# Kernel tuning notes

Hardware: AMD Instinct MI355X
Metric: run time of the kernel (lower is better)

The kernel has to match this reference:

```python
import jax, jax.numpy as jnp
import numpy as np
import math

B, L, D, H, F = 4, 2048, 1024, 16, 4096
SF = 5          # sampling_factor
EPS = 1e-12     # LayerNorm eps


def setup_inputs() -> dict:
    key = jax.random.key(0)
    ks = jax.random.split(key, 18)
    s = 0.02
    lin = lambda k, i, o: (jax.random.normal(k, (i, o), jnp.float32) * s)
    log_LK = math.ceil(math.log1p(L))
    U_part = min(SF * L * log_LK, L)  # = L here
    return {
        "x": jax.random.normal(ks[0], (B, L, D), jnp.float32),
        "wq": lin(ks[1], D, D), "bq": jnp.zeros((D,), jnp.float32),
        "wk": lin(ks[2], D, D), "bk": jnp.zeros((D,), jnp.float32),
        "wv": lin(ks[3], D, D), "bv": jnp.zeros((D,), jnp.float32),
        "wo": lin(ks[4], D, D), "bo": jnp.zeros((D,), jnp.float32),
        "w1": lin(ks[5], D, F), "b1": jnp.zeros((F,), jnp.float32),
        "w2": lin(ks[6], F, D), "b2": jnp.zeros((D,), jnp.float32),
        "gamma1": jnp.ones((D,), jnp.float32), "beta1": jnp.zeros((D,), jnp.float32),
        "gamma2": jnp.ones((D,), jnp.float32), "beta2": jnp.zeros((D,), jnp.float32),
        "index_sample": jax.random.randint(ks[7], (U_part,), 0, L, jnp.int32),
    }


def _layernorm(x, g, b):
    m = x.mean(-1, keepdims=True)
    v = ((x - m) ** 2).mean(-1, keepdims=True)  # unbiased=False
    return g * (x - m) / jnp.sqrt(v + EPS) + b


def _prob_sparse_mha(x, wq, bq, wk, bk, wv, bv, wo, bo, index_sample):
    d = D // H
    BH = B * H
    # NOTE: source views q as (B, H, L, d) WITHOUT transpose (quirk kept);
    # k, v are split with the usual (B, L, H, d) -> (B, H, L, d) transpose.
    q = (x @ wq + bq).reshape(BH, L, d)
    k = (x @ wk + bk).reshape(B, L, H, d).transpose(0, 2, 1, 3).reshape(BH, L, d)
    v = (x @ wv + bv).reshape(B, L, H, d).transpose(0, 2, 1, 3).reshape(BH, L, d)

    # --- ProbSparse query selection ---
    K_sample = k[:, index_sample, :]                       # [BH, U_part, d]
    QK = jnp.einsum('bqd,bkd->bqk', q, K_sample)           # [BH, L, U_part]
    M = QK.max(axis=-1) - QK.sum(axis=-1) / L              # sparsity measure
    u = min(SF * math.ceil(math.log1p(L)), L)              # static: 40
    _, M_top = jax.lax.top_k(-M, u)                        # largest=False in src
    Q_reduce = jnp.take_along_axis(q, M_top[:, :, None], axis=1)  # [BH, u, d]

    # --- attention for the selected queries ---
    scores = jnp.einsum('bud,bkd->buk', Q_reduce, k) / math.sqrt(d)
    probs = jax.nn.softmax(scores, axis=-1)
    out_red = jnp.einsum('buk,bkd->bud', probs, v)         # [BH, u, d]

    # scatter reduced outputs back to full length (non-selected rows -> 0)
    full = jnp.zeros_like(q).at[jnp.arange(BH)[:, None], M_top].set(out_red)
    out = full.reshape(B, H, L, d).transpose(0, 2, 1, 3).reshape(B, L, D)
    return out @ wo + bo


def reference(x, wq, bq, wk, bk, wv, bv, wo, bo, w1, b1, w2, b2,
              gamma1, beta1, gamma2, beta2, index_sample):
    a = _prob_sparse_mha(x, wq, bq, wk, bk, wv, bv, wo, bo, index_sample)
    x1 = _layernorm(x + a, gamma1, beta1)          # dropout = identity (eval)
    f = jnp.maximum(x1 @ w1 + b1, 0.0) @ w2 + b2   # FFN (ReLU)
    return _layernorm(x1 + f, gamma2, beta2)
```

## Files before the change

### kernel.cpp

```cpp
#include <hip/hip_runtime.h>
#include <float.h>
#include <math.h>

#define L_SEQ 2048
#define D_MODEL 1024
#define N_HEAD 16
#define HD 64
#define N_BH 64
#define U_TOP 40

using bf16x8 = __attribute__((ext_vector_type(8))) short;
using f32x4  = __attribute__((ext_vector_type(4))) float;

__device__ __forceinline__ unsigned short f2bf(float f) {
    unsigned int u = __builtin_bit_cast(unsigned int, f);
    u += 0x7fff + ((u >> 16) & 1);
    return (unsigned short)(u >> 16);
}
__device__ __forceinline__ float bf2f(unsigned short h) {
    unsigned int u = ((unsigned int)h) << 16;
    return __builtin_bit_cast(float, u);
}

__device__ __forceinline__ void gload_lds16(const void* g, void* l) {
    __builtin_amdgcn_global_load_lds(
        (const __attribute__((address_space(1))) unsigned int*)g,
        (__attribute__((address_space(3))) unsigned int*)l, 16, 0, 0);
}

template<bool OUTBF16, bool RELU, bool ACCUM>
__global__ void __launch_bounds__(256)
gemm_bf16(const unsigned short* __restrict__ A, int lda,
          const unsigned short* __restrict__ BT, int ldbt,
          void* __restrict__ Cp, int ldc, int K,
          const float* __restrict__ bias)
{
    __shared__ short As[4096];
    __shared__ short Bs[4096];
    const int tid = threadIdx.x;
    const int w = tid >> 6, l = tid & 63;
    const int bx = blockIdx.x, by = blockIdx.y;
    const int wm = w >> 1, wn = w & 1;

    f32x4 acc[4][4] = {};

    const unsigned short* a_src[2];
    const unsigned short* b_src[2];
#pragma unroll
    for (int g = 0; g < 2; ++g) {
        int r = w * 32 + g * 16 + (l >> 2);
        int kc = (l & 3) ^ ((r >> 1) & 3);
        a_src[g] = A + (size_t)(by * 128 + r) * lda + kc * 8;
        b_src[g] = BT + (size_t)(bx * 128 + r) * ldbt + kc * 8;
    }
    short* As_w = As + w * 1024;
    short* Bs_w = Bs + w * 1024;

    const int lr = l & 15, lg = l >> 4;

    for (int k0 = 0; k0 < K; k0 += 32) {
        __syncthreads();
        gload_lds16(a_src[0] + k0, As_w);
        gload_lds16(a_src[1] + k0, As_w + 512);
        gload_lds16(b_src[0] + k0, Bs_w);
        gload_lds16(b_src[1] + k0, Bs_w + 512);
        __syncthreads();

        bf16x8 af[4], bg[4];
#pragma unroll
        for (int m = 0; m < 4; ++m) {
            int row = wm * 64 + m * 16 + lr;
            int off = row * 64 + ((lg ^ ((row >> 1) & 3)) << 4);
            af[m] = *(const bf16x8*)((const char*)As + off);
        }
#pragma unroll
        for (int n = 0; n < 4; ++n) {
            int row = wn * 64 + n * 16 + lr;
            int off = row * 64 + ((lg ^ ((row >> 1) & 3)) << 4);
            bg[n] = *(const bf16x8*)((const char*)Bs + off);
        }
#pragma unroll
        for (int m = 0; m < 4; ++m)
#pragma unroll
            for (int n = 0; n < 4; ++n)
                acc[m][n] = __builtin_amdgcn_mfma_f32_16x16x32_bf16(
                    af[m], bg[n], acc[m][n], 0, 0, 0);
    }

    float bcol[4];
#pragma unroll
    for (int n = 0; n < 4; ++n) {
        int colg = bx * 128 + wn * 64 + n * 16 + lr;
        bcol[n] = bias ? bias[colg] : 0.f;
    }
#pragma unroll
    for (int m = 0; m < 4; ++m) {
#pragma unroll
        for (int n = 0; n < 4; ++n) {
            int colg = bx * 128 + wn * 64 + n * 16 + lr;
#pragma unroll
            for (int r = 0; r < 4; ++r) {
                int rowg = by * 128 + wm * 64 + m * 16 + lg * 4 + r;
                float v = acc[m][n][r] + bcol[n];
                if (RELU) v = fmaxf(v, 0.f);
                if (OUTBF16) {
                    ((unsigned short*)Cp)[(size_t)rowg * ldc + colg] = f2bf(v);
                } else {
                    float* C = (float*)Cp;
                    if (ACCUM) v += C[(size_t)rowg * ldc + colg];
                    C[(size_t)rowg * ldc + colg] = v;
                }
            }
        }
    }
}

__global__ void __launch_bounds__(256)
gemm_bf16_split(const unsigned short* __restrict__ Ah,
                const unsigned short* __restrict__ Al, int lda,
                const unsigned short* __restrict__ BhT,
                const unsigned short* __restrict__ BlT, int ldbt,
                unsigned short* __restrict__ CP, int K,
                const float* __restrict__ bias)
{
    __shared__ short Ash[4096], Asl[4096], Bsh[4096], Bsl[4096];
    const int tid = threadIdx.x;
    const int w = tid >> 6, l = tid & 63;
    const int bx = blockIdx.x, by = blockIdx.y;
    const int wm = w >> 1, wn = w & 1;

    f32x4 acc[4][4] = {};

    size_t a_off[2], b_off[2];
#pragma unroll
    for (int g = 0; g < 2; ++g) {
        int r = w * 32 + g * 16 + (l >> 2);
        int kc = (l & 3) ^ ((r >> 1) & 3);
        a_off[g] = (size_t)(by * 128 + r) * lda + kc * 8;
        b_off[g] = (size_t)(bx * 128 + r) * ldbt + kc * 8;
    }
    const int wb = w * 1024;
    const int lr = l & 15, lg = l >> 4;

    for (int k0 = 0; k0 < K; k0 += 32) {
        __syncthreads();
#pragma unroll
        for (int g = 0; g < 2; ++g) {
            gload_lds16(Ah + a_off[g] + k0, Ash + wb + g * 512);
            gload_lds16(Al + a_off[g] + k0, Asl + wb + g * 512);
            gload_lds16(BhT + b_off[g] + k0, Bsh + wb + g * 512);
            gload_lds16(BlT + b_off[g] + k0, Bsl + wb + g * 512);
        }
        __syncthreads();

        bf16x8 afh[4], afl[4], bgh[4], bgl[4];
#pragma unroll
        for (int m = 0; m < 4; ++m) {
            int row = wm * 64 + m * 16 + lr;
            int off = row * 64 + ((lg ^ ((row >> 1) & 3)) << 4);
            afh[m] = *(const bf16x8*)((const char*)Ash + off);
            afl[m] = *(const bf16x8*)((const char*)Asl + off);
        }
#pragma unroll
        for (int n = 0; n < 4; ++n) {
            int row = wn * 64 + n * 16 + lr;
            int off = row * 64 + ((lg ^ ((row >> 1) & 3)) << 4);
            bgh[n] = *(const bf16x8*)((const char*)Bsh + off);
            bgl[n] = *(const bf16x8*)((const char*)Bsl + off);
        }
#pragma unroll
        for (int m = 0; m < 4; ++m)
#pragma unroll
            for (int n = 0; n < 4; ++n) {
                acc[m][n] = __builtin_amdgcn_mfma_f32_16x16x32_bf16(
                    afh[m], bgh[n], acc[m][n], 0, 0, 0);
                acc[m][n] = __builtin_amdgcn_mfma_f32_16x16x32_bf16(
                    afh[m], bgl[n], acc[m][n], 0, 0, 0);
                acc[m][n] = __builtin_amdgcn_mfma_f32_16x16x32_bf16(
                    afl[m], bgh[n], acc[m][n], 0, 0, 0);
            }
    }

    float bcol[4];
#pragma unroll
    for (int n = 0; n < 4; ++n)
        bcol[n] = bias[bx * 128 + wn * 64 + n * 16 + lr];
    const int cg = bx * 2 + wn;
#pragma unroll
    for (int m = 0; m < 4; ++m)
#pragma unroll
        for (int n = 0; n < 4; ++n) {
            int cwi = n * 16 + lr;
#pragma unroll
            for (int r = 0; r < 4; ++r) {
                int rowg = by * 128 + wm * 64 + m * 16 + lg * 4 + r;
                float v = acc[m][n][r] + bcol[n];
                unsigned short hh = f2bf(v);
                unsigned short ll = f2bf(v - bf2f(hh));
                size_t ad = (size_t)rowg * 2048 + cg * 128 + cwi;
                CP[ad] = hh;
                CP[ad + 64] = ll;
            }
        }
}

__global__ void __launch_bounds__(256)
gather_ks(const unsigned short* __restrict__ KP, const int* __restrict__ idxs,
          unsigned short* __restrict__ KS)
{
    const int bh = blockIdx.x, b = bh >> 4, h = bh & 15;
    const int r0 = blockIdx.y * 256;
    const int s = threadIdx.x & 15, jr = threadIdx.x >> 4;
#pragma unroll
    for (int p = 0; p < 16; ++p) {
        int j = r0 + p * 16 + jr;
        int idx = idxs[j];
        int kc = (s & 7) ^ (j & 7);
        const unsigned short* src = KP + (size_t)(b * 2048 + idx) * 2048
                                  + h * 128 + ((s & 8) << 3) + kc * 8;
        *(bf16x8*)(KS + ((size_t)bh * 2048 + j) * 128 + s * 8) =
            *(const bf16x8*)src;
    }
}

__global__ void __launch_bounds__(256)
mstat_mfma2(const unsigned short* __restrict__ QP,
            const unsigned short* __restrict__ KS,
            float* __restrict__ Mout)
{
    __shared__ char lds[32768];
    const int tid = threadIdx.x, w = tid >> 6, l = tid & 63;
    const int bh = blockIdx.x, qt = blockIdx.y;
    const int i0 = qt * 256;
    const int lr = l & 15, lg = l >> 4;

    bf16x8 af[4][2][2];
#pragma unroll
    for (int half = 0; half < 2; ++half) {
        __syncthreads();
#pragma unroll
        for (int it = 0; it < 8; ++it) {
            int rq = w * 64 + it * 8 + (l >> 3);
            int i = i0 + rq;
            int kc = (l & 7) ^ (rq & 7);
            gload_lds16(QP + (size_t)(bh * 128 + (i >> 4)) * 2048
                           + (i & 15) * 128 + half * 64 + kc * 8,
                        lds + w * 8192 + it * 1024);
        }
        __syncthreads();
#pragma unroll
        for (int m = 0; m < 4; ++m) {
            int rq = w * 64 + m * 16 + lr;
#pragma unroll
            for (int ks = 0; ks < 2; ++ks) {
                int c = (ks * 4 + lg) ^ (rq & 7);
                af[m][ks][half] = *(const bf16x8*)(lds + rq * 128 + (c << 4));
            }
        }
    }
    __syncthreads();

    float mx[4][4], sm[4][4];
#pragma unroll
    for (int m = 0; m < 4; ++m)
#pragma unroll
        for (int r = 0; r < 4; ++r) { mx[m][r] = -FLT_MAX; sm[m][r] = 0.f; }

    const unsigned short* ksbase = KS + (size_t)bh * (2048 * 128);

#pragma unroll
    for (int it = 0; it < 4; ++it)
        gload_lds16(ksbase + w * 2048 + it * 512 + l * 8,
                    lds + w * 4096 + it * 1024);

    for (int jt = 0; jt < 32; ++jt) {
        const int cur = jt & 1;
        __syncthreads();
        if (jt + 1 < 32) {
#pragma unroll
            for (int it = 0; it < 4; ++it)
                gload_lds16(ksbase + (size_t)(jt + 1) * 8192 + w * 2048 + it * 512 + l * 8,
                            lds + (cur ^ 1) * 16384 + w * 4096 + it * 1024);
        }
        const char* kb = lds + cur * 16384;
#pragma unroll
        for (int n = 0; n < 4; ++n) {
            int jr = n * 16 + lr;
            bf16x8 bgh[2], bgl[2];
#pragma unroll
            for (int ks = 0; ks < 2; ++ks) {
                int c = (ks * 4 + lg) ^ (jr & 7);
                bgh[ks] = *(const bf16x8*)(kb + jr * 256 + (c << 4));
                bgl[ks] = *(const bf16x8*)(kb + jr * 256 + (c << 4) + 128);
            }
#pragma unroll
            for (int m = 0; m < 4; ++m) {
                f32x4 a = {};
                a = __builtin_amdgcn_mfma_f32_16x16x32_bf16(af[m][0][0], bgh[0], a, 0, 0, 0);
                a = __builtin_amdgcn_mfma_f32_16x16x32_bf16(af[m][0][1], bgh[0], a, 0, 0, 0);
                a = __builtin_amdgcn_mfma_f32_16x16x32_bf16(af[m][0][0], bgl[0], a, 0, 0, 0);
                a = __builtin_amdgcn_mfma_f32_16x16x32_bf16(af[m][1][0], bgh[1], a, 0, 0, 0);
                a = __builtin_amdgcn_mfma_f32_16x16x32_bf16(af[m][1][1], bgh[1], a, 0, 0, 0);
                a = __builtin_amdgcn_mfma_f32_16x16x32_bf16(af[m][1][0], bgl[1], a, 0, 0, 0);
#pragma unroll
                for (int r = 0; r < 4; ++r) {
                    mx[m][r] = fmaxf(mx[m][r], a[r]);
                    sm[m][r] += a[r];
                }
            }
        }
    }

#pragma unroll
    for (int m = 0; m < 4; ++m)
#pragma unroll
        for (int r = 0; r < 4; ++r) {
            float a = mx[m][r], s = sm[m][r];
#pragma unroll
            for (int mask = 1; mask < 16; mask <<= 1) {
                a = fmaxf(a, __shfl_xor(a, mask));
                s += __shfl_xor(s, mask);
            }
            if (lr == 0) {
                int row = i0 + w * 64 + m * 16 + lg * 4 + r;
                Mout[(size_t)bh * L_SEQ + row] = a - s * (1.0f / 2048.0f);
            }
        }
}

__global__ void __launch_bounds__(256)
tconv(const float* __restrict__ in, int R, int C, unsigned short* __restrict__ out)
{
    __shared__ float t[32][33];
    const int bx = blockIdx.x * 32;
    const int by = blockIdx.y * 32;
    const int lx = threadIdx.x & 31, ly = threadIdx.x >> 5;
#pragma unroll
    for (int r = 0; r < 4; ++r)
        t[ly + r * 8][lx] = in[(size_t)(by + ly + r * 8) * C + bx + lx];
    __syncthreads();
#pragma unroll
    for (int r = 0; r < 4; ++r) {
        int oc = ly + r * 8;
        out[(size_t)(bx + oc) * R + by + lx] = f2bf(t[lx][oc]);
    }
}

__global__ void __launch_bounds__(256)
tconv_split(const float* __restrict__ in, int R, int C,
            unsigned short* __restrict__ outh, unsigned short* __restrict__ outl)
{
    __shared__ float t[32][33];
    const int bx = blockIdx.x * 32;
    const int by = blockIdx.y * 32;
    const int lx = threadIdx.x & 31, ly = threadIdx.x >> 5;
#pragma unroll
    for (int r = 0; r < 4; ++r)
        t[ly + r * 8][lx] = in[(size_t)(by + ly + r * 8) * C + bx + lx];
    __syncthreads();
#pragma unroll
    for (int r = 0; r < 4; ++r) {
        int oc = ly + r * 8;
        float f = t[lx][oc];
        unsigned short hh = f2bf(f);
        outh[(size_t)(bx + oc) * R + by + lx] = hh;
        outl[(size_t)(bx + oc) * R + by + lx] = f2bf(f - bf2f(hh));
    }
}

__global__ void __launch_bounds__(256)
split_f32(const float* __restrict__ in, unsigned short* __restrict__ hi,
          unsigned short* __restrict__ lo)
{
    size_t i = ((size_t)blockIdx.x * 256 + threadIdx.x) * 4;
    float4 v = *(const float4*)(in + i);
    ushort4 h, l2;
    h.x = f2bf(v.x); l2.x = f2bf(v.x - bf2f(h.x));
    h.y = f2bf(v.y); l2.y = f2bf(v.y - bf2f(h.y));
    h.z = f2bf(v.z); l2.z = f2bf(v.z - bf2f(h.z));
    h.w = f2bf(v.w); l2.w = f2bf(v.w - bf2f(h.w));
    *(ushort4*)(hi + i) = h;
    *(ushort4*)(lo + i) = l2;
}

__global__ void __launch_bounds__(256)
topk_kernel(const float* __restrict__ M, int* __restrict__ Mtop)
{
    __shared__ float mv[L_SEQ];
    __shared__ float wv_[4];
    __shared__ int wi_[4];
    const int bh = blockIdx.x;
    const int tid = threadIdx.x;
    for (int j = tid; j < L_SEQ; j += 256) mv[j] = M[(size_t)bh * L_SEQ + j];
    __syncthreads();
    for (int u = 0; u < U_TOP; ++u) {
        float best = FLT_MAX;
        int bi = 1 << 30;
        for (int j = tid; j < L_SEQ; j += 256) {
            float v = mv[j];
            if (v < best || (v == best && j < bi)) { best = v; bi = j; }
        }
#pragma unroll
        for (int off = 32; off; off >>= 1) {
            float ov = __shfl_down(best, off);
            int oi = __shfl_down(bi, off);
            if (ov < best || (ov == best && oi < bi)) { best = ov; bi = oi; }
        }
        if ((tid & 63) == 0) { wv_[tid >> 6] = best; wi_[tid >> 6] = bi; }
        __syncthreads();
        if (tid == 0) {
            for (int w = 1; w < 4; ++w)
                if (wv_[w] < best || (wv_[w] == best && wi_[w] < bi)) { best = wv_[w]; bi = wi_[w]; }
            Mtop[bh * U_TOP + u] = bi;
            mv[bi] = FLT_MAX;
        }
        __syncthreads();
    }
}

__global__ void __launch_bounds__(256)
attn_fused(const unsigned short* __restrict__ QP,
           const unsigned short* __restrict__ KP,
           const unsigned short* __restrict__ V,
           const int* __restrict__ Mtop,
           unsigned short* __restrict__ OUTC)
{
    __shared__ unsigned short Qs[64 * 64];
    __shared__ unsigned short Ks[128 * 64];
    __shared__ unsigned short Vt[64 * 128];
    __shared__ unsigned short Pb[64 * 128];
    const int bh = blockIdx.x;
    const int b = bh >> 4, h = bh & 15;
    const int tid = threadIdx.x, w = tid >> 6, l = tid & 63;
    const int lr = l & 15, lg = l >> 4;

#pragma unroll
    for (int is = 0; is < 2; ++is) {
        int row = w * 16 + is * 8 + (l >> 3);
        int u = row < U_TOP ? row : U_TOP - 1;
        int lsel = Mtop[bh * U_TOP + u];
        int cg = (l & 7) ^ (row & 7);
        gload_lds16(QP + (size_t)(bh * 128 + (lsel >> 4)) * 2048
                       + (lsel & 15) * 128 + cg * 8,
                    &Qs[(w * 16 + is * 8) * 64]);
    }
    __syncthreads();

    bf16x8 af[2];
    {
        int row = w * 16 + lr;
#pragma unroll
        for (int ks = 0; ks < 2; ++ks) {
            int c = (ks * 4 + lg) ^ (row & 7);
            af[ks] = *(const bf16x8*)((const char*)Qs + row * 128 + (c << 4));
        }
    }

    float m_run[4], l_run[4];
    f32x4 oacc[4] = {};
#pragma unroll
    for (int r = 0; r < 4; ++r) { m_run[r] = -FLT_MAX; l_run[r] = 0.f; }

    for (int t = 0; t < 16; ++t) {
        const int j0 = t * 128;
        __syncthreads();

#pragma unroll
        for (int is = 0; is < 4; ++is) {
            int kr = w * 32 + is * 8 + (l >> 3);
            int cg = (l & 7) ^ (kr & 7);
            gload_lds16(KP + (size_t)(b * 2048 + j0 + kr) * 2048 + h * 128 + cg * 8,
                        &Ks[(w * 32 + is * 8) * 64]);
        }
        {
            int key = tid & 127, dh = (tid >> 7) * 32;
            const unsigned short* vsrc =
                V + (((size_t)(b * L_SEQ + j0 + key)) << 10) + (h << 6) + dh;
            bf16x8 vv[4];
#pragma unroll
            for (int i = 0; i < 4; ++i) vv[i] = *(const bf16x8*)(vsrc + i * 8);
            int ck = key >> 3, klo = (key & 7) * 2;
#pragma unroll
            for (int i = 0; i < 4; ++i)
#pragma unroll
                for (int j = 0; j < 8; ++j) {
                    int d = dh + i * 8 + j;
                    *(unsigned short*)((char*)Vt + d * 256 +
                                       ((ck ^ (d & 7)) << 4) + klo) =
                        (unsigned short)vv[i][j];
                }
        }
        __syncthreads();

        f32x4 sc[8] = {};
#pragma unroll
        for (int ks = 0; ks < 2; ++ks)
#pragma unroll
            for (int n = 0; n < 8; ++n) {
                int krow = n * 16 + lr;
                int c = (ks * 4 + lg) ^ (krow & 7);
                bf16x8 bf = *(const bf16x8*)((const char*)Ks + krow * 128 + (c << 4));
                sc[n] = __builtin_amdgcn_mfma_f32_16x16x32_bf16(af[ks], bf, sc[n], 0, 0, 0);
            }

        float rs[4];
#pragma unroll
        for (int r = 0; r < 4; ++r) {
            int row = w * 16 + lg * 4 + r;
            float mt = -FLT_MAX;
#pragma unroll
            for (int n = 0; n < 8; ++n) mt = fmaxf(mt, sc[n][r]);
            mt *= 0.125f;
#pragma unroll
            for (int mask = 1; mask < 16; mask <<= 1)
                mt = fmaxf(mt, __shfl_xor(mt, mask));
            float mn = fmaxf(m_run[r], mt);
            rs[r] = expf(m_run[r] - mn);
            float ls = 0.f;
            int rsw = row & 7;
#pragma unroll
            for (int n = 0; n < 8; ++n) {
                float p = expf(sc[n][r] * 0.125f - mn);
                ls += p;
                int ckp = (lr >> 3) + 2 * n;
                *(unsigned short*)((char*)Pb + row * 256 +
                                   ((ckp ^ rsw) << 4) + (lr & 7) * 2) = f2bf(p);
            }
#pragma unroll
            for (int mask = 1; mask < 16; mask <<= 1) ls += __shfl_xor(ls, mask);
            l_run[r] = l_run[r] * rs[r] + ls;
            m_run[r] = mn;
        }
        __syncthreads();

#pragma unroll
        for (int n = 0; n < 4; ++n)
#pragma unroll
            for (int r = 0; r < 4; ++r) oacc[n][r] *= rs[r];
#pragma unroll
        for (int ks = 0; ks < 4; ++ks) {
            int arow = w * 16 + lr;
            int ca = (lg + ks * 4) ^ (arow & 7);
            bf16x8 pa = *(const bf16x8*)((const char*)Pb + arow * 256 + (ca << 4));
#pragma unroll
            for (int n = 0; n < 4; ++n) {
                int d = n * 16 + lr;
                int cb = (lg + ks * 4) ^ (d & 7);
                bf16x8 vb = *(const bf16x8*)((const char*)Vt + d * 256 + (cb << 4));
                oacc[n] = __builtin_amdgcn_mfma_f32_16x16x32_bf16(pa, vb, oacc[n], 0, 0, 0);
            }
        }
    }

#pragma unroll
    for (int r = 0; r < 4; ++r) {
        int row = w * 16 + lg * 4 + r;
        float inv = 1.f / l_run[r];
#pragma unroll
        for (int n = 0; n < 4; ++n)
            OUTC[bh * 4096 + row * 64 + n * 16 + lr] = f2bf(oacc[n][r] * inv);
    }
}

__global__ void __launch_bounds__(256)
woscatter(const unsigned short* __restrict__ OUTC,
          const unsigned short* __restrict__ woT,
          const int* __restrict__ Mtop,
          float* __restrict__ Ab)
{
    const int bh = blockIdx.x, b = bh >> 4, h = bh & 15;
    const int tid = threadIdx.x, w = tid >> 6, l = tid & 63;
    const int lr = l & 15, lg = l >> 4;

    bf16x8 af[3][2];
#pragma unroll
    for (int m = 0; m < 3; ++m)
#pragma unroll
        for (int ks = 0; ks < 2; ++ks)
            af[m][ks] = *(const bf16x8*)(OUTC + bh * 4096 + (m * 16 + lr) * 64
                                         + (ks * 4 + lg) * 8);
    int lsel[3][4];
#pragma unroll
    for (int m = 0; m < 3; ++m)
#pragma unroll
        for (int r = 0; r < 4; ++r) {
            int row = m * 16 + lg * 4 + r;
            lsel[m][r] = row < U_TOP ? Mtop[bh * U_TOP + row] : -1;
        }

    for (int nn = 0; nn < 16; ++nn) {
        int ng = w * 16 + nn;
        bf16x8 bg[2];
#pragma unroll
        for (int ks = 0; ks < 2; ++ks)
            bg[ks] = *(const bf16x8*)(woT + (size_t)(ng * 16 + lr) * 1024
                                      + h * 64 + (ks * 4 + lg) * 8);
        f32x4 a[3] = {};
#pragma unroll
        for (int m = 0; m < 3; ++m)
#pragma unroll
            for (int ks = 0; ks < 2; ++ks)
                a[m] = __builtin_amdgcn_mfma_f32_16x16x32_bf16(af[m][ks], bg[ks], a[m], 0, 0, 0);
#pragma unroll
        for (int m = 0; m < 3; ++m)
#pragma unroll
            for (int r = 0; r < 4; ++r)
                if (lsel[m][r] >= 0)
                    atomicAdd(Ab + (size_t)(b * 2048 + lsel[m][r]) * 1024
                              + ng * 16 + lr, a[m][r]);
    }
}

template<bool WB16, bool BADD>
__global__ void __launch_bounds__(256)
ln_kernel(const float* __restrict__ X, const float* __restrict__ A,
          const float* __restrict__ badd,
          const float* __restrict__ g, const float* __restrict__ be,
          float* __restrict__ out, unsigned short* __restrict__ out16)
{
    __shared__ float wred[4];
    const int row = blockIdx.x, tid = threadIdx.x;
    float4 xv = *(const float4*)(X + (size_t)row * D_MODEL + tid * 4);
    float4 av = *(const float4*)(A + (size_t)row * D_MODEL + tid * 4);
    float v0 = xv.x + av.x, v1 = xv.y + av.y, v2 = xv.z + av.z, v3 = xv.w + av.w;
    if (BADD) {
        float4 bb = *(const float4*)(badd + tid * 4);
        v0 += bb.x; v1 += bb.y; v2 += bb.z; v3 += bb.w;
    }

    float s = v0 + v1 + v2 + v3;
#pragma unroll
    for (int off = 32; off; off >>= 1) s += __shfl_down(s, off);
    if ((tid & 63) == 0) wred[tid >> 6] = s;
    __syncthreads();
    float mean = (wred[0] + wred[1] + wred[2] + wred[3]) * (1.f / 1024.f);
    __syncthreads();

    float d0 = v0 - mean, d1 = v1 - mean, d2 = v2 - mean, d3 = v3 - mean;
    float q = d0 * d0 + d1 * d1 + d2 * d2 + d3 * d3;
#pragma unroll
    for (int off = 32; off; off >>= 1) q += __shfl_down(q, off);
    if ((tid & 63) == 0) wred[tid >> 6] = q;
    __syncthreads();
    float var = (wred[0] + wred[1] + wred[2] + wred[3]) * (1.f / 1024.f);
    float rstd = rsqrtf(var + 1e-12f);

    float4 gv = *(const float4*)(g + tid * 4);
    float4 bv = *(const float4*)(be + tid * 4);
    float4 o;
    o.x = gv.x * d0 * rstd + bv.x;
    o.y = gv.y * d1 * rstd + bv.y;
    o.z = gv.z * d2 * rstd + bv.z;
    o.w = gv.w * d3 * rstd + bv.w;
    *(float4*)(out + (size_t)row * D_MODEL + tid * 4) = o;
    if (WB16) {
        ushort4 ob;
        ob.x = f2bf(o.x); ob.y = f2bf(o.y); ob.z = f2bf(o.z); ob.w = f2bf(o.w);
        *(ushort4*)(out16 + (size_t)row * D_MODEL + tid * 4) = ob;
    }
}

extern "C" void kernel_launch(void* const* d_in, const int* in_sizes, int n_in,
                              void* d_out, int out_size, void* d_ws, size_t ws_size,
                              hipStream_t stream)
{
    const float* x   = (const float*)d_in[0];
    const float* wq  = (const float*)d_in[1];
    const float* bq  = (const float*)d_in[2];
    const float* wk  = (const float*)d_in[3];
    const float* bk  = (const float*)d_in[4];
    const float* wv  = (const float*)d_in[5];
    const float* bv  = (const float*)d_in[6];
    const float* wo  = (const float*)d_in[7];
    const float* bo  = (const float*)d_in[8];
    const float* w1  = (const float*)d_in[9];
    const float* b1  = (const float*)d_in[10];
    const float* w2  = (const float*)d_in[11];
    const float* b2  = (const float*)d_in[12];
    const float* g1  = (const float*)d_in[13];
    const float* be1 = (const float*)d_in[14];
    const float* g2  = (const float*)d_in[15];
    const float* be2 = (const float*)d_in[16];
    const int*  idxs = (const int*)d_in[17];

    char* ws  = (char*)d_ws;
    char* dob = (char*)d_out;
    const size_t MB = 1u << 20;

    unsigned short* QP   = (unsigned short*)(ws);
    unsigned short* KP   = (unsigned short*)(ws + 32 * MB);
    unsigned short* xh   = (unsigned short*)(ws + 64 * MB);
    unsigned short* xl   = (unsigned short*)(ws + 80 * MB);
    unsigned short* KS   = (unsigned short*)(ws + 64 * MB);
    float*          Ab   = (float*)(ws + 64 * MB);
    float*          x1f  = (float*)(ws + 96 * MB);
    unsigned short* x1b  = (unsigned short*)(ws);
    unsigned short* w1T  = (unsigned short*)(ws + 16 * MB);
    unsigned short* w2T  = (unsigned short*)(ws + 24 * MB);
    unsigned short* HIDc = (unsigned short*)(ws + 32 * MB);

    unsigned short* woT  = (unsigned short*)(dob);
    unsigned short* wqhT = (unsigned short*)(dob + 2 * MB);
    unsigned short* wqlT = (unsigned short*)(dob + 4 * MB);
    unsigned short* wkhT = (unsigned short*)(dob + 6 * MB);
    unsigned short* wklT = (unsigned short*)(dob + 8 * MB);
    unsigned short* wvT  = (unsigned short*)(dob + 10 * MB);
    float*          Mb   = (float*)(dob + 12 * MB);
    int*            Mtop = (int*)(dob + 12 * MB + 768 * 1024);
    unsigned short* Vb   = (unsigned short*)(dob + 13 * MB);
    unsigned short* OUTC = (unsigned short*)(dob + 29 * MB);
    float*          F    = (float*)d_out;

    dim3 blk(256);
    dim3 g_gemm(8, 64);

    split_f32<<<dim3(8192), blk, 0, stream>>>(x, xh, xl);
    tconv_split<<<dim3(32, 32), blk, 0, stream>>>(wq, 1024, 1024, wqhT, wqlT);
    tconv_split<<<dim3(32, 32), blk, 0, stream>>>(wk, 1024, 1024, wkhT, wklT);
    tconv<<<dim3(32, 32), blk, 0, stream>>>(wv, 1024, 1024, wvT);
    tconv<<<dim3(32, 32), blk, 0, stream>>>(wo, 1024, 1024, woT);

    gemm_bf16_split<<<g_gemm, blk, 0, stream>>>(xh, xl, 1024, wqhT, wqlT, 1024,
                                                QP, 1024, bq);
    gemm_bf16_split<<<g_gemm, blk, 0, stream>>>(xh, xl, 1024, wkhT, wklT, 1024,
                                                KP, 1024, bk);
    gemm_bf16<true, false, false><<<g_gemm, blk, 0, stream>>>(xh, 1024, wvT, 1024,
                                                              Vb, 1024, 1024, bv);

    gather_ks<<<dim3(64, 8), blk, 0, stream>>>(KP, idxs, KS);
    mstat_mfma2<<<dim3(64, 8), blk, 0, stream>>>(QP, KS, Mb);
    topk_kernel<<<dim3(64), blk, 0, stream>>>(Mb, Mtop);

    hipMemsetAsync(Ab, 0, 32 * MB, stream);
    attn_fused<<<dim3(N_BH), blk, 0, stream>>>(QP, KP, Vb, Mtop, OUTC);
    woscatter<<<dim3(N_BH), blk, 0, stream>>>(OUTC, woT, Mtop, Ab);

    ln_kernel<true, true><<<dim3(8192), blk, 0, stream>>>(x, Ab, bo, g1, be1, x1f, x1b);

    tconv<<<dim3(128, 32), blk, 0, stream>>>(w1, 1024, 4096, w1T);
    tconv<<<dim3(32, 128), blk, 0, stream>>>(w2, 4096, 1024, w2T);

    for (int c = 0; c < 2; ++c) {
        gemm_bf16<true, true, false><<<dim3(16, 64), blk, 0, stream>>>(
            x1b, 1024, w1T + (size_t)c * 2048 * 1024, 1024, HIDc, 2048, 1024, b1 + c * 2048);
        if (c == 0)
            gemm_bf16<false, false, false><<<g_gemm, blk, 0, stream>>>(
                HIDc, 2048, w2T + c * 2048, 4096, F, 1024, 2048, b2);
        else
            gemm_bf16<false, false, true><<<g_gemm, blk, 0, stream>>>(
                HIDc, 2048, w2T + c * 2048, 4096, F, 1024, 2048, nullptr);
    }

    ln_kernel<false, false><<<dim3(8192), blk, 0, stream>>>(x1f, F, nullptr, g2, be2,
                                                            (float*)d_out, nullptr);
}
```

Baseline: 840.0 us.

## Split attention over key chunks, fuse preprocessing, shrink mstat tiles, unchunk FFN

Four preprocessing kernels are merged into one launch. The mstat kernel now processes 128 query rows per block instead of 256, doubling its grid. Attention is split four ways across key chunks per head, flash-decoding style: partial outputs and max/sum stats go to a buffer and are merged in woscatter before the Wo projection. The FFN now runs as one full-width GEMM pair instead of two chunks. The aim is more parallelism from the 64-block attention kernel and fewer launches. The cost is extra partial-output traffic and the merge arithmetic in woscatter.

```diff
diff --git a/kernel.cpp b/kernel.cpp
--- a/kernel.cpp
+++ b/kernel.cpp
@@ -205,6 +205,69 @@
 }
 
 __global__ void __launch_bounds__(256)
+preprocess(const float* __restrict__ x,
+           const float* __restrict__ wq, const float* __restrict__ wk,
+           const float* __restrict__ wv, const float* __restrict__ wo,
+           unsigned short* __restrict__ xh, unsigned short* __restrict__ xl,
+           unsigned short* __restrict__ wqhT, unsigned short* __restrict__ wqlT,
+           unsigned short* __restrict__ wkhT, unsigned short* __restrict__ wklT,
+           unsigned short* __restrict__ wvT, unsigned short* __restrict__ woT)
+{
+    __shared__ float t[32][33];
+    const int bid = blockIdx.x, tid = threadIdx.x;
+    if (bid < 8192) {
+        size_t i = (size_t)bid * 1024 + tid * 4;
+        float4 v = *(const float4*)(x + i);
+        ushort4 h, l2;
+        h.x = f2bf(v.x); l2.x = f2bf(v.x - bf2f(h.x));
+        h.y = f2bf(v.y); l2.y = f2bf(v.y - bf2f(h.y));
+        h.z = f2bf(v.z); l2.z = f2bf(v.z - bf2f(h.z));
+        h.w = f2bf(v.w); l2.w = f2bf(v.w - bf2f(h.w));
+        *(ushort4*)(xh + i) = h;
+        *(ushort4*)(xl + i) = l2;
+        return;
+    }
+    const int grp = (bid - 8192) >> 10;
+    const int b2 = (bid - 8192) & 1023;
+    const int bx = (b2 & 31) * 32, by = (b2 >> 5) * 32;
+    const float* in = (grp == 0) ? wq : (grp == 1) ? wk : (grp == 2) ? wv : wo;
+    const int lx = tid & 31, ly = tid >> 5;
+#pragma unroll
+    for (int r = 0; r < 4; ++r)
+        t[ly + r * 8][lx] = in[(size_t)(by + ly + r * 8) * 1024 + bx + lx];
+    __syncthreads();
+#pragma unroll
+    for (int r = 0; r < 4; ++r) {
+        int oc = ly + r * 8;
+        float f = t[lx][oc];
+        size_t od = (size_t)(bx + oc) * 1024 + by + lx;
+        unsigned short hh = f2bf(f);
+        if (grp == 0) { wqhT[od] = hh; wqlT[od] = f2bf(f - bf2f(hh)); }
+        else if (grp == 1) { wkhT[od] = hh; wklT[od] = f2bf(f - bf2f(hh)); }
+        else if (grp == 2) wvT[od] = hh;
+        else woT[od] = hh;
+    }
+}
+
+__global__ void __launch_bounds__(256)
+tconv(const float* __restrict__ in, int R, int C, unsigned short* __restrict__ out)
+{
+    __shared__ float t[32][33];
+    const int bx = blockIdx.x * 32;
+    const int by = blockIdx.y * 32;
+    const int lx = threadIdx.x & 31, ly = threadIdx.x >> 5;
+#pragma unroll
+    for (int r = 0; r < 4; ++r)
+        t[ly + r * 8][lx] = in[(size_t)(by + ly + r * 8) * C + bx + lx];
+    __syncthreads();
+#pragma unroll
+    for (int r = 0; r < 4; ++r) {
+        int oc = ly + r * 8;
+        out[(size_t)(bx + oc) * R + by + lx] = f2bf(t[lx][oc]);
+    }
+}
+
+__global__ void __launch_bounds__(256)
 gather_ks(const unsigned short* __restrict__ KP, const int* __restrict__ idxs,
           unsigned short* __restrict__ KS)
 {
@@ -231,26 +294,26 @@
     __shared__ char lds[32768];
     const int tid = threadIdx.x, w = tid >> 6, l = tid & 63;
     const int bh = blockIdx.x, qt = blockIdx.y;
-    const int i0 = qt * 256;
+    const int i0 = qt * 128;
     const int lr = l & 15, lg = l >> 4;
 
-    bf16x8 af[4][2][2];
+    bf16x8 af[2][2][2];
 #pragma unroll
     for (int half = 0; half < 2; ++half) {
         __syncthreads();
 #pragma unroll
-        for (int it = 0; it < 8; ++it) {
-            int rq = w * 64 + it * 8 + (l >> 3);
+        for (int it = 0; it < 4; ++it) {
+            int rq = w * 32 + it * 8 + (l >> 3);
             int i = i0 + rq;
             int kc = (l & 7) ^ (rq & 7);
             gload_lds16(QP + (size_t)(bh * 128 + (i >> 4)) * 2048
                            + (i & 15) * 128 + half * 64 + kc * 8,
-                        lds + w * 8192 + it * 1024);
-        }
-        __syncthreads();
-#pragma unroll
-        for (int m = 0; m < 4; ++m) {
-            int rq = w * 64 + m * 16 + lr;
+                        lds + w * 4096 + it * 1024);
+        }
+        __syncthreads();
+#pragma unroll
+        for (int m = 0; m < 2; ++m) {
+            int rq = w * 32 + m * 16 + lr;
 #pragma unroll
             for (int ks = 0; ks < 2; ++ks) {
                 int c = (ks * 4 + lg) ^ (rq & 7);
@@ -260,9 +323,9 @@
     }
     __syncthreads();
 
-    float mx[4][4], sm[4][4];
-#pragma unroll
-    for (int m = 0; m < 4; ++m)
+    float mx[2][4], sm[2][4];
+#pragma unroll
+    for (int m = 0; m < 2; ++m)
 #pragma unroll
         for (int r = 0; r < 4; ++r) { mx[m][r] = -FLT_MAX; sm[m][r] = 0.f; }
 
@@ -294,7 +357,7 @@
                 bgl[ks] = *(const bf16x8*)(kb + jr * 256 + (c << 4) + 128);
             }
 #pragma unroll
-            for (int m = 0; m < 4; ++m) {
+            for (int m = 0; m < 2; ++m) {
                 f32x4 a = {};
                 a = __builtin_amdgcn_mfma_f32_16x16x32_bf16(af[m][0][0], bgh[0], a, 0, 0, 0);
                 a = __builtin_amdgcn_mfma_f32_16x16x32_bf16(af[m][0][1], bgh[0], a, 0, 0, 0);
@@ -312,7 +375,7 @@
     }
 
 #pragma unroll
-    for (int m = 0; m < 4; ++m)
+    for (int m = 0; m < 2; ++m)
 #pragma unroll
         for (int r = 0; r < 4; ++r) {
             float a = mx[m][r], s = sm[m][r];
@@ -322,65 +385,10 @@
                 s += __shfl_xor(s, mask);
             }
             if (lr == 0) {
-                int row = i0 + w * 64 + m * 16 + lg * 4 + r;
+                int row = i0 + w * 32 + m * 16 + lg * 4 + r;
                 Mout[(size_t)bh * L_SEQ + row] = a - s * (1.0f / 2048.0f);
             }
         }
-}
-
-__global__ void __launch_bounds__(256)
-tconv(const float* __restrict__ in, int R, int C, unsigned short* __restrict__ out)
-{
-    __shared__ float t[32][33];
-    const int bx = blockIdx.x * 32;
-    const int by = blockIdx.y * 32;
-    const int lx = threadIdx.x & 31, ly = threadIdx.x >> 5;
-#pragma unroll
-    for (int r = 0; r < 4; ++r)
-        t[ly + r * 8][lx] = in[(size_t)(by + ly + r * 8) * C + bx + lx];
-    __syncthreads();
-#pragma unroll
-    for (int r = 0; r < 4; ++r) {
-        int oc = ly + r * 8;
-        out[(size_t)(bx + oc) * R + by + lx] = f2bf(t[lx][oc]);
-    }
-}
-
-__global__ void __launch_bounds__(256)
-tconv_split(const float* __restrict__ in, int R, int C,
-            unsigned short* __restrict__ outh, unsigned short* __restrict__ outl)
-{
-    __shared__ float t[32][33];
-    const int bx = blockIdx.x * 32;
-    const int by = blockIdx.y * 32;
-    const int lx = threadIdx.x & 31, ly = threadIdx.x >> 5;
-#pragma unroll
-    for (int r = 0; r < 4; ++r)
-        t[ly + r * 8][lx] = in[(size_t)(by + ly + r * 8) * C + bx + lx];
-    __syncthreads();
-#pragma unroll
-    for (int r = 0; r < 4; ++r) {
-        int oc = ly + r * 8;
-        float f = t[lx][oc];
-        unsigned short hh = f2bf(f);
-        outh[(size_t)(bx + oc) * R + by + lx] = hh;
-        outl[(size_t)(bx + oc) * R + by + lx] = f2bf(f - bf2f(hh));
-    }
-}
-
-__global__ void __launch_bounds__(256)
-split_f32(const float* __restrict__ in, unsigned short* __restrict__ hi,
-          unsigned short* __restrict__ lo)
-{
-    size_t i = ((size_t)blockIdx.x * 256 + threadIdx.x) * 4;
-    float4 v = *(const float4*)(in + i);
-    ushort4 h, l2;
-    h.x = f2bf(v.x); l2.x = f2bf(v.x - bf2f(h.x));
-    h.y = f2bf(v.y); l2.y = f2bf(v.y - bf2f(h.y));
-    h.z = f2bf(v.z); l2.z = f2bf(v.z - bf2f(h.z));
-    h.w = f2bf(v.w); l2.w = f2bf(v.w - bf2f(h.w));
-    *(ushort4*)(hi + i) = h;
-    *(ushort4*)(lo + i) = l2;
 }
 
 __global__ void __launch_bounds__(256)
@@ -423,13 +431,14 @@
            const unsigned short* __restrict__ KP,
            const unsigned short* __restrict__ V,
            const int* __restrict__ Mtop,
-           unsigned short* __restrict__ OUTC)
+           unsigned short* __restrict__ PART,
+           float* __restrict__ ML)
 {
     __shared__ unsigned short Qs[64 * 64];
     __shared__ unsigned short Ks[128 * 64];
     __shared__ unsigned short Vt[64 * 128];
     __shared__ unsigned short Pb[64 * 128];
-    const int bh = blockIdx.x;
+    const int sp = blockIdx.x, bh = blockIdx.y;
     const int b = bh >> 4, h = bh & 15;
     const int tid = threadIdx.x, w = tid >> 6, l = tid & 63;
     const int lr = l & 15, lg = l >> 4;
@@ -461,7 +470,7 @@
 #pragma unroll
     for (int r = 0; r < 4; ++r) { m_run[r] = -FLT_MAX; l_run[r] = 0.f; }
 
-    for (int t = 0; t < 16; ++t) {
+    for (int t = sp * 4; t < sp * 4 + 4; ++t) {
         const int j0 = t * 128;
         __syncthreads();
 
@@ -552,18 +561,23 @@
         }
     }
 
+    const int pbase = (bh * 4 + sp) * 64;
 #pragma unroll
     for (int r = 0; r < 4; ++r) {
         int row = w * 16 + lg * 4 + r;
-        float inv = 1.f / l_run[r];
 #pragma unroll
         for (int n = 0; n < 4; ++n)
-            OUTC[bh * 4096 + row * 64 + n * 16 + lr] = f2bf(oacc[n][r] * inv);
-    }
-}
-
-__global__ void __launch_bounds__(256)
-woscatter(const unsigned short* __restrict__ OUTC,
+            PART[(size_t)(pbase + row) * 64 + n * 16 + lr] = f2bf(oacc[n][r]);
+        if (lr == 0) {
+            ML[(size_t)(pbase + row) * 2 + 0] = m_run[r];
+            ML[(size_t)(pbase + row) * 2 + 1] = l_run[r];
+        }
+    }
+}
+
+__global__ void __launch_bounds__(256)
+woscatter(const unsigned short* __restrict__ PART,
+          const float* __restrict__ ML,
           const unsigned short* __restrict__ woT,
           const int* __restrict__ Mtop,
           float* __restrict__ Ab)
@@ -574,11 +588,37 @@
 
     bf16x8 af[3][2];
 #pragma unroll
-    for (int m = 0; m < 3; ++m)
-#pragma unroll
-        for (int ks = 0; ks < 2; ++ks)
-            af[m][ks] = *(const bf16x8*)(OUTC + bh * 4096 + (m * 16 + lr) * 64
-                                         + (ks * 4 + lg) * 8);
+    for (int m = 0; m < 3; ++m) {
+        int row = m * 16 + lr;
+        float ms[4], ls[4];
+#pragma unroll
+        for (int s = 0; s < 4; ++s) {
+            ms[s] = ML[(size_t)((bh * 4 + s) * 64 + row) * 2 + 0];
+            ls[s] = ML[(size_t)((bh * 4 + s) * 64 + row) * 2 + 1];
+        }
+        float M = fmaxf(fmaxf(ms[0], ms[1]), fmaxf(ms[2], ms[3]));
+        float wgt[4], L = 0.f;
+#pragma unroll
+        for (int s = 0; s < 4; ++s) { wgt[s] = expf(ms[s] - M); L += wgt[s] * ls[s]; }
+        float invL = 1.f / L;
+#pragma unroll
+        for (int ks = 0; ks < 2; ++ks) {
+            float a8[8] = {};
+#pragma unroll
+            for (int s = 0; s < 4; ++s) {
+                bf16x8 po = *(const bf16x8*)(PART +
+                    (size_t)((bh * 4 + s) * 64 + row) * 64 + (ks * 4 + lg) * 8);
+#pragma unroll
+                for (int j = 0; j < 8; ++j)
+                    a8[j] += wgt[s] * bf2f((unsigned short)po[j]);
+            }
+            bf16x8 fr;
+#pragma unroll
+            for (int j = 0; j < 8; ++j) fr[j] = (short)f2bf(a8[j] * invL);
+            af[m][ks] = fr;
+        }
+    }
+
     int lsel[3][4];
 #pragma unroll
     for (int m = 0; m < 3; ++m)
@@ -697,7 +737,7 @@
     unsigned short* x1b  = (unsigned short*)(ws);
     unsigned short* w1T  = (unsigned short*)(ws + 16 * MB);
     unsigned short* w2T  = (unsigned short*)(ws + 24 * MB);
-    unsigned short* HIDc = (unsigned short*)(ws + 32 * MB);
+    unsigned short* HID  = (unsigned short*)(ws + 32 * MB);
 
     unsigned short* woT  = (unsigned short*)(dob);
     unsigned short* wqhT = (unsigned short*)(dob + 2 * MB);
@@ -708,17 +748,16 @@
     float*          Mb   = (float*)(dob + 12 * MB);
     int*            Mtop = (int*)(dob + 12 * MB + 768 * 1024);
     unsigned short* Vb   = (unsigned short*)(dob + 13 * MB);
-    unsigned short* OUTC = (unsigned short*)(dob + 29 * MB);
+    unsigned short* PART = (unsigned short*)(dob + 29 * MB);
+    float*          ML   = (float*)(dob + 31 * MB);
     float*          F    = (float*)d_out;
 
     dim3 blk(256);
     dim3 g_gemm(8, 64);
 
-    split_f32<<<dim3(8192), blk, 0, stream>>>(x, xh, xl);
-    tconv_split<<<dim3(32, 32), blk, 0, stream>>>(wq, 1024, 1024, wqhT, wqlT);
-    tconv_split<<<dim3(32, 32), blk, 0, stream>>>(wk, 1024, 1024, wkhT, wklT);
-    tconv<<<dim3(32, 32), blk, 0, stream>>>(wv, 1024, 1024, wvT);
-    tconv<<<dim3(32, 32), blk, 0, stream>>>(wo, 1024, 1024, woT);
+    preprocess<<<dim3(12288), blk, 0, stream>>>(x, wq, wk, wv, wo,
+                                                xh, xl, wqhT, wqlT, wkhT, wklT,
+                                                wvT, woT);
 
     gemm_bf16_split<<<g_gemm, blk, 0, stream>>>(xh, xl, 1024, wqhT, wqlT, 1024,
                                                 QP, 1024, bq);
@@ -728,28 +767,22 @@
                                                               Vb, 1024, 1024, bv);
 
     gather_ks<<<dim3(64, 8), blk, 0, stream>>>(KP, idxs, KS);
-    mstat_mfma2<<<dim3(64, 8), blk, 0, stream>>>(QP, KS, Mb);
+    mstat_mfma2<<<dim3(64, 16), blk, 0, stream>>>(QP, KS, Mb);
     topk_kernel<<<dim3(64), blk, 0, stream>>>(Mb, Mtop);
 
     hipMemsetAsync(Ab, 0, 32 * MB, stream);
-    attn_fused<<<dim3(N_BH), blk, 0, stream>>>(QP, KP, Vb, Mtop, OUTC);
-    woscatter<<<dim3(N_BH), blk, 0, stream>>>(OUTC, woT, Mtop, Ab);
+    attn_fused<<<dim3(4, N_BH), blk, 0, stream>>>(QP, KP, Vb, Mtop, PART, ML);
+    woscatter<<<dim3(N_BH), blk, 0, stream>>>(PART, ML, woT, Mtop, Ab);
 
     ln_kernel<true, true><<<dim3(8192), blk, 0, stream>>>(x, Ab, bo, g1, be1, x1f, x1b);
 
     tconv<<<dim3(128, 32), blk, 0, stream>>>(w1, 1024, 4096, w1T);
     tconv<<<dim3(32, 128), blk, 0, stream>>>(w2, 4096, 1024, w2T);
 
-    for (int c = 0; c < 2; ++c) {
-        gemm_bf16<true, true, false><<<dim3(16, 64), blk, 0, stream>>>(
-            x1b, 1024, w1T + (size_t)c * 2048 * 1024, 1024, HIDc, 2048, 1024, b1 + c * 2048);
-        if (c == 0)
-            gemm_bf16<false, false, false><<<g_gemm, blk, 0, stream>>>(
-                HIDc, 2048, w2T + c * 2048, 4096, F, 1024, 2048, b2);
-        else
-            gemm_bf16<false, false, true><<<g_gemm, blk, 0, stream>>>(
-                HIDc, 2048, w2T + c * 2048, 4096, F, 1024, 2048, nullptr);
-    }
+    gemm_bf16<true, true, false><<<dim3(32, 64), blk, 0, stream>>>(
+        x1b, 1024, w1T, 1024, HID, 4096, 1024, b1);
+    gemm_bf16<false, false, false><<<g_gemm, blk, 0, stream>>>(
+        HID, 4096, w2T, 4096, F, 1024, 4096, b2);
 
     ln_kernel<false, false><<<dim3(8192), blk, 0, stream>>>(x1f, F, nullptr, g2, be2,
                                                             (float*)d_out, nullptr);
```

Result: faster. 751.2 us (-10.6%).
